# Optimization experiments

Measured on AMD Instinct MI355X. Metric: run time of the kernel, lower is better.

The kernel has to match this reference:

```python
import jax, jax.numpy as jnp
import numpy as np

MARGIN = 0.3
NORM = 2.0  # p-norm used by both pairwise() and PairwiseDistance

M, C = 65536, 256   # n*h*w pixels, feature channels
K, P, Q = 20, 2048, 2048  # classes 1..nclass-1, positives, negatives per class


def setup_inputs() -> dict:
    key = jax.random.key(0)
    k1, k2, k3 = jax.random.split(key, 3)
    features = jax.random.normal(k1, (M, C), dtype=jnp.float32)
    pos_idx = jax.random.randint(k2, (K, P), 0, M)
    neg_idx = jax.random.randint(k3, (K, Q), 0, M)
    return {"features": features, "pos_idx": pos_idx, "neg_idx": neg_idx}


def _pairwise(x, y):
    # torch: clamp(xx - 2xy + yy, 0); (dis + eps) ** (1/norm)
    eps = 0.0001 / x.shape[1]
    xx = jnp.sum(x * x, axis=1)           # [P]
    yy = jnp.sum(y * y, axis=1)           # [Q]
    xy = x @ y.T                           # [P,Q] GEMM
    dis = jnp.clip(xx[:, None] - 2.0 * xy + yy[None, :], 0.0)
    return (dis + eps) ** (1.0 / NORM)


def _pdist(x1, x2):
    # PairwiseDistance: (clamp(sum(|x1-x2|^p), 0) + eps) ** (1/p)
    eps = 0.0001 / x1.shape[1]
    out = jnp.sum(jnp.abs(x1 - x2) ** NORM, axis=1)
    return (jnp.clip(out, 0.0) + eps) ** (1.0 / NORM)


def _class_loss(pos, neg):
    # hard mining on detached features (indices only, as in generate_triplet_simple)
    pos_d = jax.lax.stop_gradient(pos)
    neg_d = jax.lax.stop_gradient(neg)
    hp = jnp.argmax(_pairwise(pos_d, pos_d), axis=1)   # hardest positive per anchor
    hn = jnp.argmin(_pairwise(pos_d, neg_d), axis=1)   # hardest negative per anchor
    d_p = _pdist(pos, pos[hp])
    d_n = _pdist(pos, neg[hn])
    return jnp.mean(jnp.clip(MARGIN + d_p - d_n, 0.0))


def reference(features, pos_idx, neg_idx):
    f = jax.nn.sigmoid(features)          # torch.sigmoid(features)
    pos = f[pos_idx]                      # [K,P,C]
    neg = f[neg_idx]                      # [K,Q,C]
    losses = jax.vmap(_class_loss)(pos, neg)  # per-class triplet losses
    return jnp.sum(losses)                # loss accumulated over classes
```

## Files before the change

kernel.cpp:

```cpp
#include <hip/hip_runtime.h>
#include <stdint.h>

#define M_ROWS 65536
#define C_DIM  256
#define K_CLS  20
#define P_POS  2048
#define MARGIN_F 0.3f
#define EPS_D (0.0001f / 256.0f)
#define SCALE1 0x7F7F7F7Fu
#define SCALE2 0x80808080u

typedef float floatx4 __attribute__((ext_vector_type(4)));
typedef int   intx8   __attribute__((ext_vector_type(8)));
union Frag8 { intx8 v; uint4 q[2]; };

__device__ __forceinline__ void async_copy16(const void* g, void* l) {
    __builtin_amdgcn_global_load_lds(
        (const __attribute__((address_space(1))) void*)g,
        (__attribute__((address_space(3))) void*)l, 16, 0, 0);
}
__device__ __forceinline__ float sigm(float x) { return 1.f / (1.f + __expf(-x)); }

__device__ __forceinline__ void negA(Frag8& f) {
#pragma unroll
    for (int t = 0; t < 8; ++t) f.v[t] ^= (int)0x80808080u;
}

__global__ __launch_bounds__(256) void sigmoid_norm_k(
        const float* __restrict__ feat,
        unsigned int* __restrict__ S8,
        float* __restrict__ xx,
        unsigned int* __restrict__ hp,
        unsigned int* __restrict__ hn) {
    {
        const int idx = blockIdx.x * 256 + threadIdx.x;
        if (idx < K_CLS * P_POS) { hp[idx] = 0u; hn[idx] = 0xFFFFFFFFu; }
    }
    const int wave = threadIdx.x >> 6, lane = threadIdx.x & 63;
    const int row = blockIdx.x * 4 + wave;
    const float4 v = *(const float4*)(feat + (size_t)row * C_DIM + lane * 4);

    const int p01 = __builtin_amdgcn_cvt_pk_fp8_f32(sigm(v.x), sigm(v.y), 0, false);
    const int p23 = __builtin_amdgcn_cvt_pk_fp8_f32(sigm(v.z), sigm(v.w), 0, false);
    const unsigned int packed = (unsigned int)(p01 & 0xFFFF) | ((unsigned int)p23 << 16);
    S8[(size_t)row * 64 + lane] = packed;

    const float q0 = __builtin_amdgcn_cvt_f32_fp8(p01, 0);
    const float q1 = __builtin_amdgcn_cvt_f32_fp8(p01, 1);
    const float q2 = __builtin_amdgcn_cvt_f32_fp8(p23, 0);
    const float q3 = __builtin_amdgcn_cvt_f32_fp8(p23, 1);
    float sum = q0 * q0 + q1 * q1 + q2 * q2 + q3 * q3;
#pragma unroll
    for (int off = 32; off; off >>= 1) sum += __shfl_down(sum, off);
    if (lane == 0) xx[row] = sum;
}

__global__ __launch_bounds__(256, 3) void select_k(
        const unsigned int* __restrict__ S8,
        const float* __restrict__ xx,
        const int* __restrict__ pos_idx,
        const int* __restrict__ neg_idx,
        unsigned int* __restrict__ hp,
        unsigned int* __restrict__ hn) {
    __shared__ __align__(16) unsigned char Bt[2][32 * 256];
    __shared__ float yyL[512];

    const int tid    = threadIdx.x;
    const int w      = tid >> 6;
    const int lane   = tid & 63;
    const int lane15 = lane & 15;
    const int quad   = lane >> 4;

    const int bid    = blockIdx.x;
    const int ctid   = bid % 40;
    const int rest   = bid / 40;
    const int i_blk  = rest >> 2;
    const int jq     = rest & 3;
    const int k      = ctid >> 1;
    const int isNeg  = ctid & 1;
    const int i0     = i_blk * 256;
    const int j0     = jq * 512;

    const int* __restrict__ idxA = pos_idx + k * P_POS;
    const int* __restrict__ idxB = (isNeg ? neg_idx : pos_idx) + k * P_POS;
    unsigned int* outKey         = (isNeg ? hn : hp) + k * P_POS;

    const char* S8B = (const char*)S8;

    const int rl  = lane >> 4;
    const int cch = lane & 15;
    int rloc[2], soff[2];
#pragma unroll
    for (int c = 0; c < 2; ++c) {
        rloc[c] = (w * 2 + c) * 4 + rl;
        soff[c] = (cch ^ (rloc[c] & 15)) << 4;
    }

    int g_st[2];
#pragma unroll
    for (int c = 0; c < 2; ++c) g_st[c] = idxB[j0 + rloc[c]];
#pragma unroll
    for (int c = 0; c < 2; ++c)
        async_copy16(S8B + ((size_t)(uint32_t)g_st[c] << 8) + soff[c],
                     (char*)&Bt[0][0] + (w * 2 + c) * 1024);
#pragma unroll
    for (int c = 0; c < 2; ++c) g_st[c] = idxB[j0 + 32 + rloc[c]];

#pragma unroll
    for (int t = 0; t < 2; ++t) {
        const int jj = t * 256 + tid;
        yyL[jj] = xx[idxB[j0 + jj]];
    }

    Frag8 A_reg[4][2];
#pragma unroll
    for (int si = 0; si < 4; ++si) {
        const int gi = idxA[i0 + w * 64 + si * 16 + lane15];
        const char* rb = S8B + ((size_t)(uint32_t)gi << 8) + quad * 32;
#pragma unroll
        for (int s = 0; s < 2; ++s) {
            A_reg[si][s].q[0] = *(const uint4*)(rb + s * 128);
            A_reg[si][s].q[1] = *(const uint4*)(rb + s * 128 + 16);
            negA(A_reg[si][s]);
        }
    }

    int blo[2], bhi[2];
#pragma unroll
    for (int s = 0; s < 2; ++s) {
        const int c0 = s * 8 + quad * 2;
        blo[s] = lane15 * 256 + ((c0 ^ lane15) << 4);
        bhi[s] = lane15 * 256 + (((c0 + 1) ^ lane15) << 4);
    }

    float bestv[16];
    const float binit = isNeg ? 3.4e38f : -3.4e38f;
#pragma unroll
    for (int t = 0; t < 16; ++t) bestv[t] = binit;

#pragma unroll 2
    for (int jc = 0; jc < 16; ++jc) {
        __syncthreads();

        const float yv0 = yyL[(jc << 5) + lane15];
        const float yv1 = yyL[(jc << 5) + 16 + lane15];

        if (jc < 15) {
            char* lb = (char*)(&Bt[(jc + 1) & 1][0]);
#pragma unroll
            for (int c = 0; c < 2; ++c)
                async_copy16(S8B + ((size_t)(uint32_t)g_st[c] << 8) + soff[c],
                             lb + (w * 2 + c) * 1024);
        }
        {
            const int nt = j0 + (jc < 14 ? jc + 2 : 15) * 32;
#pragma unroll
            for (int c = 0; c < 2; ++c) g_st[c] = idxB[nt + rloc[c]];
        }

        const char* Bb = (const char*)(&Bt[jc & 1][0]);
        const floatx4 yv4_0 = {yv0, yv0, yv0, yv0};
        const floatx4 yv4_1 = {yv1, yv1, yv1, yv1};
        floatx4 acc[2][4];
        {
            Frag8 bf0, bf1;
            bf0.q[0] = *(const uint4*)(Bb + blo[0]);
            bf0.q[1] = *(const uint4*)(Bb + bhi[0]);
            bf1.q[0] = *(const uint4*)(Bb + blo[0] + 4096);
            bf1.q[1] = *(const uint4*)(Bb + bhi[0] + 4096);
#pragma unroll
            for (int si = 0; si < 4; ++si)
                acc[0][si] = __builtin_amdgcn_mfma_scale_f32_16x16x128_f8f6f4(
                    A_reg[si][0].v, bf0.v, yv4_0, 0, 0,
                    0, SCALE2, 0, SCALE1);
#pragma unroll
            for (int si = 0; si < 4; ++si)
                acc[1][si] = __builtin_amdgcn_mfma_scale_f32_16x16x128_f8f6f4(
                    A_reg[si][0].v, bf1.v, yv4_1, 0, 0,
                    0, SCALE2, 0, SCALE1);
        }
        {
            Frag8 bf0, bf1;
            bf0.q[0] = *(const uint4*)(Bb + blo[1]);
            bf0.q[1] = *(const uint4*)(Bb + bhi[1]);
            bf1.q[0] = *(const uint4*)(Bb + blo[1] + 4096);
            bf1.q[1] = *(const uint4*)(Bb + bhi[1] + 4096);
#pragma unroll
            for (int si = 0; si < 4; ++si)
                acc[0][si] = __builtin_amdgcn_mfma_scale_f32_16x16x128_f8f6f4(
                    A_reg[si][1].v, bf0.v, acc[0][si], 0, 0,
                    0, SCALE2, 0, SCALE1);
#pragma unroll
            for (int si = 0; si < 4; ++si)
                acc[1][si] = __builtin_amdgcn_mfma_scale_f32_16x16x128_f8f6f4(
                    A_reg[si][1].v, bf1.v, acc[1][si], 0, 0,
                    0, SCALE2, 0, SCALE1);
        }

        const uint32_t jb0 = (uint32_t)((j0 + (jc << 5)) | lane15);
        const uint32_t jb1 = jb0 | 16u;
#pragma unroll
        for (int si = 0; si < 4; ++si)
#pragma unroll
            for (int r = 0; r < 4; ++r) {
                const float e0 = __uint_as_float(
                    (__float_as_uint(acc[0][si][r]) & 0xFFFFF800u) | jb0);
                const float e1 = __uint_as_float(
                    (__float_as_uint(acc[1][si][r]) & 0xFFFFF800u) | jb1);
                const int slot = si * 4 + r;
                bestv[slot] = isNeg ? fminf(fminf(bestv[slot], e0), e1)
                                    : fmaxf(fmaxf(bestv[slot], e0), e1);
            }
    }

#pragma unroll
    for (int slot = 0; slot < 16; ++slot) {
#pragma unroll
        for (int off = 1; off < 16; off <<= 1) {
            const float ov = __shfl_xor(bestv[slot], off);
            bestv[slot] = isNeg ? fminf(bestv[slot], ov) : fmaxf(bestv[slot], ov);
        }
    }
    if (lane15 == 0) {
#pragma unroll
        for (int si = 0; si < 4; ++si)
#pragma unroll
            for (int r = 0; r < 4; ++r) {
                const int row = w * 64 + si * 16 + quad * 4 + r;
                const uint32_t u = __float_as_uint(bestv[si * 4 + r]);
                const uint32_t key = (u & 0x80000000u) ? ~u : (u | 0x80000000u);
                if (isNeg) atomicMin(&outKey[i0 + row], key);
                else       atomicMax(&outKey[i0 + row], key);
            }
    }
}

#define ACC16(UA, UP, UN)                                                     \
    {                                                                         \
        float xa, d;                                                          \
        xa = __builtin_amdgcn_cvt_f32_fp8((int)(UA), 0);                      \
        d = xa - __builtin_amdgcn_cvt_f32_fp8((int)(UP), 0); dp += d * d;     \
        d = xa - __builtin_amdgcn_cvt_f32_fp8((int)(UN), 0); dn += d * d;     \
        xa = __builtin_amdgcn_cvt_f32_fp8((int)(UA), 1);                      \
        d = xa - __builtin_amdgcn_cvt_f32_fp8((int)(UP), 1); dp += d * d;     \
        d = xa - __builtin_amdgcn_cvt_f32_fp8((int)(UN), 1); dn += d * d;     \
        xa = __builtin_amdgcn_cvt_f32_fp8((int)(UA), 2);                      \
        d = xa - __builtin_amdgcn_cvt_f32_fp8((int)(UP), 2); dp += d * d;     \
        d = xa - __builtin_amdgcn_cvt_f32_fp8((int)(UN), 2); dn += d * d;     \
        xa = __builtin_amdgcn_cvt_f32_fp8((int)(UA), 3);                      \
        d = xa - __builtin_amdgcn_cvt_f32_fp8((int)(UP), 3); dp += d * d;     \
        d = xa - __builtin_amdgcn_cvt_f32_fp8((int)(UN), 3); dn += d * d;     \
    }

__global__ __launch_bounds__(256) void loss_k(
        const unsigned int* __restrict__ S8,
        const int* __restrict__ pos_idx,
        const int* __restrict__ neg_idx,
        const unsigned int* __restrict__ hp,
        const unsigned int* __restrict__ hn,
        float* __restrict__ terms) {
    const int tid    = threadIdx.x;
    const int lane15 = tid & 15;
    const int grp    = tid >> 4;
    const int a      = blockIdx.x * 16 + grp;
    const int k      = a >> 11;
    const int i      = a & 2047;
    const int* pidx = pos_idx + (k << 11);
    const int* nidx = neg_idx + (k << 11);
    const unsigned int kp = hp[a], kn = hn[a];
    const int jp = (int)((kp & 0x80000000u) ? (kp & 2047u) : ((~kp) & 2047u));
    const int jn = (int)((kn & 0x80000000u) ? (kn & 2047u) : ((~kn) & 2047u));
    const int ga = pidx[i];
    const int gp = pidx[jp];
    const int gn = nidx[jn];

    const char* S8B = (const char*)S8;
    const uint4 va = *(const uint4*)(S8B + ((size_t)(uint32_t)ga << 8) + lane15 * 16);
    const uint4 vp = *(const uint4*)(S8B + ((size_t)(uint32_t)gp << 8) + lane15 * 16);
    const uint4 vn = *(const uint4*)(S8B + ((size_t)(uint32_t)gn << 8) + lane15 * 16);

    float dp = 0.f, dn = 0.f;
    ACC16(va.x, vp.x, vn.x)
    ACC16(va.y, vp.y, vn.y)
    ACC16(va.z, vp.z, vn.z)
    ACC16(va.w, vp.w, vn.w)

#pragma unroll
    for (int off = 1; off < 16; off <<= 1) {
        dp += __shfl_xor(dp, off);
        dn += __shfl_xor(dn, off);
    }
    if (lane15 == 0) {
        const float d_p = sqrtf(fmaxf(dp, 0.f) + EPS_D);
        const float d_n = sqrtf(fmaxf(dn, 0.f) + EPS_D);
        terms[a] = fmaxf(MARGIN_F + d_p - d_n, 0.f);
    }
}

__global__ __launch_bounds__(1024) void reduce_k(
        const float* __restrict__ terms, float* __restrict__ out) {
    __shared__ float red[1024];
    float s = 0.f;
    for (int i = threadIdx.x; i < K_CLS * P_POS; i += 1024) s += terms[i];
    red[threadIdx.x] = s;
    __syncthreads();
    for (int off = 512; off; off >>= 1) {
        if ((int)threadIdx.x < off) red[threadIdx.x] += red[threadIdx.x + off];
        __syncthreads();
    }
    if (threadIdx.x == 0) out[0] = red[0] * (1.0f / (float)P_POS);
}

extern "C" void kernel_launch(void* const* d_in, const int* in_sizes, int n_in,
                              void* d_out, int out_size, void* d_ws, size_t ws_size,
                              hipStream_t stream) {
    const float* feat    = (const float*)d_in[0];
    const int*   pos_idx = (const int*)d_in[1];
    const int*   neg_idx = (const int*)d_in[2];

    char* ws = (char*)d_ws;
    unsigned int* S8 = (unsigned int*)ws;
    float*        xx = (float*)(ws + 16777216);
    unsigned int* hp = (unsigned int*)(ws + 17039360);
    unsigned int* hn = (unsigned int*)(ws + 17203200);
    float*     terms = (float*)(ws + 17367040);

    sigmoid_norm_k<<<M_ROWS / 4, 256, 0, stream>>>(feat, S8, xx, hp, hn);

    select_k<<<32 * 40, 256, 0, stream>>>(S8, xx, pos_idx, neg_idx, hp, hn);

    loss_k<<<(K_CLS * P_POS) / 16, 256, 0, stream>>>(S8, pos_idx, neg_idx, hp, hn, terms);

    reduce_k<<<1, 1024, 0, stream>>>(terms, (float*)d_out);
}
```

Measured before the change: 179.8 us.

## Triple-buffer B tiles with two-ahead prefetch and preloaded packed gather indices

Switches the B-tile staging buffer from double to triple buffering, issuing async global-to-LDS copies two chunks ahead. A single explicit vmcnt wait plus raw s_barrier replaces the full __syncthreads per iteration. All 16 gather indices per thread are loaded up front and packed as 16-bit pairs into registers, taking the dependent index load off the loop's critical path. This adds LDS use (three 8 KB buffers), which may lower occupancy. It fully unrolls the loop, and the 16-bit packing relies on row indices being below 65536.

```diff
diff --git a/kernel.cpp b/kernel.cpp
--- a/kernel.cpp
+++ b/kernel.cpp
@@ -25,6 +25,9 @@
 #pragma unroll
     for (int t = 0; t < 8; ++t) f.v[t] ^= (int)0x80808080u;
 }
+
+#define VMCNT2() asm volatile("s_waitcnt vmcnt(2)" ::: "memory")
+#define VMCNT0() asm volatile("s_waitcnt vmcnt(0)" ::: "memory")
 
 __global__ __launch_bounds__(256) void sigmoid_norm_k(
         const float* __restrict__ feat,
@@ -62,7 +65,7 @@
         const int* __restrict__ neg_idx,
         unsigned int* __restrict__ hp,
         unsigned int* __restrict__ hn) {
-    __shared__ __align__(16) unsigned char Bt[2][32 * 256];
+    __shared__ __align__(16) unsigned char Bt[3][32 * 256];
     __shared__ float yyL[512];
 
     const int tid    = threadIdx.x;
@@ -96,15 +99,13 @@
         soff[c] = (cch ^ (rloc[c] & 15)) << 4;
     }
 
-    int g_st[2];
-#pragma unroll
-    for (int c = 0; c < 2; ++c) g_st[c] = idxB[j0 + rloc[c]];
-#pragma unroll
-    for (int c = 0; c < 2; ++c)
-        async_copy16(S8B + ((size_t)(uint32_t)g_st[c] << 8) + soff[c],
-                     (char*)&Bt[0][0] + (w * 2 + c) * 1024);
-#pragma unroll
-    for (int c = 0; c < 2; ++c) g_st[c] = idxB[j0 + 32 + rloc[c]];
+    uint32_t g_pk[16];
+#pragma unroll
+    for (int t = 0; t < 16; ++t) {
+        const uint32_t a0 = (uint32_t)idxB[j0 + t * 32 + rloc[0]];
+        const uint32_t a1 = (uint32_t)idxB[j0 + t * 32 + rloc[1]];
+        g_pk[t] = (a0 & 0xFFFFu) | (a1 << 16);
+    }
 
 #pragma unroll
     for (int t = 0; t < 2; ++t) {
@@ -133,32 +134,39 @@
         bhi[s] = lane15 * 256 + (((c0 + 1) ^ lane15) << 4);
     }
 
+#pragma unroll
+    for (int t = 0; t < 2; ++t) {
+        char* lb = (char*)&Bt[t][0] + (w * 2) * 1024;
+        async_copy16(S8B + ((size_t)(g_pk[t] & 0xFFFFu) << 8) + soff[0], lb);
+        async_copy16(S8B + ((size_t)(g_pk[t] >> 16) << 8) + soff[1], lb + 1024);
+    }
+
     float bestv[16];
     const float binit = isNeg ? 3.4e38f : -3.4e38f;
 #pragma unroll
     for (int t = 0; t < 16; ++t) bestv[t] = binit;
 
-#pragma unroll 2
+    __syncthreads();
+
+#pragma unroll
     for (int jc = 0; jc < 16; ++jc) {
-        __syncthreads();
+        if (jc) {
+            if (jc == 15) VMCNT0(); else VMCNT2();
+            __builtin_amdgcn_s_barrier();
+            __builtin_amdgcn_sched_barrier(0);
+        }
 
         const float yv0 = yyL[(jc << 5) + lane15];
         const float yv1 = yyL[(jc << 5) + 16 + lane15];
 
-        if (jc < 15) {
-            char* lb = (char*)(&Bt[(jc + 1) & 1][0]);
-#pragma unroll
-            for (int c = 0; c < 2; ++c)
-                async_copy16(S8B + ((size_t)(uint32_t)g_st[c] << 8) + soff[c],
-                             lb + (w * 2 + c) * 1024);
-        }
-        {
-            const int nt = j0 + (jc < 14 ? jc + 2 : 15) * 32;
-#pragma unroll
-            for (int c = 0; c < 2; ++c) g_st[c] = idxB[nt + rloc[c]];
-        }
-
-        const char* Bb = (const char*)(&Bt[jc & 1][0]);
+        if (jc < 14) {
+            const uint32_t pk = g_pk[jc + 2];
+            char* lb = (char*)&Bt[(jc + 2) % 3][0] + (w * 2) * 1024;
+            async_copy16(S8B + ((size_t)(pk & 0xFFFFu) << 8) + soff[0], lb);
+            async_copy16(S8B + ((size_t)(pk >> 16) << 8) + soff[1], lb + 1024);
+        }
+
+        const char* Bb = (const char*)&Bt[jc % 3][0];
         const floatx4 yv4_0 = {yv0, yv0, yv0, yv0};
         const floatx4 yv4_1 = {yv1, yv1, yv1, yv1};
         floatx4 acc[2][4];
```

After: 168.9 us. 1.06x faster.
